# Performance work log

Measured on AMD Instinct MI355X. Metric: run time of the kernel, lower is better.

Reference implementation:

```python
import jax, jax.numpy as jnp
import numpy as np

N = 50          # n_nodes
TAU = 1.0       # sinkhorn_tau
ITERS = 5       # sinkhorn_iters
ALPHA = 1.0


def _psi_fn(x, W1, b1, W2, b2):
    # x: [B, N, F]
    h = jax.nn.leaky_relu(x @ W1 + b1)          # [B, N, H], slope 0.01 matches torch default
    M = jax.nn.leaky_relu(h @ W2 + b2)          # [B, N, N]
    P = jnp.exp(M / TAU)
    for _ in range(ITERS):                      # alternating row/col normalization
        P = P / jnp.sum(P, axis=2, keepdims=True)
        P = P / jnp.sum(P, axis=1, keepdims=True)
    return P


def _hungarian(cost):
    """O(n^3) Hungarian (shortest augmenting path, like scipy.linear_sum_assignment).
    cost: [n, n] numpy. Returns col index assigned to each row (minimizes cost)."""
    n = cost.shape[0]
    INF = 1e18
    u = np.zeros(n + 1)
    v = np.zeros(n + 1)
    p = np.zeros(n + 1, dtype=np.int64)   # p[j] = row matched to column j (1-based)
    for i in range(1, n + 1):
        p[0] = i
        j0 = 0
        minv = np.full(n + 1, INF)
        way = np.zeros(n + 1, dtype=np.int64)
        used = np.zeros(n + 1, dtype=bool)
        while True:
            used[j0] = True
            i0 = p[j0]
            cur = cost[i0 - 1, :] - u[i0] - v[1:]
            free = ~used[1:]
            better = free & (cur < minv[1:])
            mv = minv[1:]
            mv[better] = cur[better]
            way[1:][better] = j0
            cand = np.where(free, mv, INF)
            j1 = int(np.argmin(cand)) + 1
            delta = cand[j1 - 1]
            u[p[used]] += delta
            v[used] -= delta
            mv[free] -= delta
            j0 = j1
            if p[j0] == 0:
                break
        while j0 != 0:
            j1 = way[j0]
            p[j0] = p[j1]
            j0 = j1
    row_to_col = np.zeros(n, dtype=np.int64)
    for j in range(1, n + 1):
        if p[j] > 0:
            row_to_col[p[j] - 1] = j - 1
    return row_to_col


def setup_inputs() -> dict:
    key = jax.random.key(0)
    k1, k2, k3, k4, k5 = jax.random.split(key, 5)
    B, F, H = 128, 1024, 4096
    s1 = 1.0 / np.sqrt(F)
    s2 = 1.0 / np.sqrt(H)
    x = jax.random.normal(k1, (B, N, F), dtype=jnp.float32)
    W1 = jax.random.uniform(k2, (F, H), minval=-s1, maxval=s1, dtype=jnp.float32)
    b1 = jax.random.uniform(k3, (H,), minval=-s1, maxval=s1, dtype=jnp.float32)
    W2 = jax.random.uniform(k4, (H, N), minval=-s2, maxval=s2, dtype=jnp.float32)
    b2 = jax.random.uniform(k5, (N,), minval=-s2, maxval=s2, dtype=jnp.float32)
    return {"x": x, "W1": W1, "b1": b1, "W2": W2, "b2": b2, "do_round": 1}


def reference(x, W1, b1, W2, b2, do_round):
    psi = _psi_fn(x, W1, b1, W2, b2)            # [B, N, N] doubly-stochastic (approx)
    if do_round:
        batch = np.asarray(psi)
        B = batch.shape[0]
        perms_np = np.zeros((B, N, N), dtype=np.float32)
        rows = np.arange(N)
        for i in range(B):
            cols = _hungarian(-batch[i])        # maximize psi == minimize -psi
            perms_np[i, rows, cols] = 1.0
        perms = jnp.asarray(perms_np)
        dist = jnp.sum(psi * perms, axis=(1, 2)) / N   # [B]
        X = (1.0 - ALPHA) * perms + ALPHA * psi
        return (psi, perms, X, dist)
    return (psi, None, None, None)
```

## Files before the change

kernel.cpp:

```cpp
#include <hip/hip_runtime.h>

#define NMAT 50
#define BATCH 128
#define FDIM 1024
#define HDIM 4096
#define ROWS 6400
#define PSIZE 320000
#define NPART 32
#define HINF 1e18

#define WS_M_OFF   0
#define WS_XH_OFF  40960000LL
#define WS_XL_OFF  54067200LL
#define WS_W1H_OFF 67174400LL
#define WS_W1L_OFF 75563008LL
#define WS_W2H_OFF 83951616LL
#define WS_W2L_OFF 84475904LL
#define WS_H_OFF   85000192LL
#define WS_MIN     (WS_H_OFF + 128LL * HDIM * 4)

typedef __bf16 bf16x8 __attribute__((ext_vector_type(8)));
typedef short short8 __attribute__((ext_vector_type(8)));
typedef float f32x4 __attribute__((ext_vector_type(4)));
typedef unsigned short u16;
typedef unsigned int u32;

__device__ __forceinline__ float bf16_to_f32(unsigned short h) {
  return __uint_as_float(((unsigned int)h) << 16);
}
__device__ __forceinline__ unsigned short f32_to_bf16(float f) {
  unsigned int u = __float_as_uint(f);
  u += 0x7FFFu + ((u >> 16) & 1u);
  return (unsigned short)(u >> 16);
}

__device__ __forceinline__ void gload16(const u16* g, u16* l) {
  __builtin_amdgcn_global_load_lds(
      (const __attribute__((address_space(1))) unsigned int*)g,
      (__attribute__((address_space(3))) unsigned int*)l, 16, 0, 0);
}

__device__ __forceinline__ double wave_min_f64(double x) {
  union { double d; int i[2]; } u, t;
  u.d = x;
#define DPP_MIN_STEP(ctrl)                                                   \
  t.i[0] = __builtin_amdgcn_update_dpp(u.i[0], u.i[0], ctrl, 0xf, 0xf, false);\
  t.i[1] = __builtin_amdgcn_update_dpp(u.i[1], u.i[1], ctrl, 0xf, 0xf, false);\
  u.d = fmin(u.d, t.d);
  DPP_MIN_STEP(0x111)
  DPP_MIN_STEP(0x112)
  DPP_MIN_STEP(0x114)
  DPP_MIN_STEP(0x118)
  DPP_MIN_STEP(0x142)
  DPP_MIN_STEP(0x143)
#undef DPP_MIN_STEP
  union { double d; int i[2]; } r;
  r.i[0] = __builtin_amdgcn_readlane(u.i[0], 63);
  r.i[1] = __builtin_amdgcn_readlane(u.i[1], 63);
  return r.d;
}

__device__ __forceinline__ float wave_min_f32(float x) {
  float t;
#define DPP_MINF_STEP(ctrl)                                                  \
  t = __uint_as_float(__builtin_amdgcn_update_dpp(                           \
      (int)__float_as_uint(x), (int)__float_as_uint(x), ctrl, 0xf, 0xf, false));\
  x = fminf(x, t);
  DPP_MINF_STEP(0x111)
  DPP_MINF_STEP(0x112)
  DPP_MINF_STEP(0x114)
  DPP_MINF_STEP(0x118)
  DPP_MINF_STEP(0x142)
  DPP_MINF_STEP(0x143)
#undef DPP_MINF_STEP
  return __uint_as_float(__builtin_amdgcn_readlane((int)__float_as_uint(x), 63));
}

__device__ __forceinline__ double readlane_f64(double x, int l) {
  union { double d; int i2[2]; } a, b;
  a.d = x;
  b.i2[0] = __builtin_amdgcn_readlane(a.i2[0], l);
  b.i2[1] = __builtin_amdgcn_readlane(a.i2[1], l);
  return b.d;
}

__global__ __launch_bounds__(256) void convert_all(
    const float* __restrict__ X, u16* __restrict__ Xh, u16* __restrict__ Xl,
    const float* __restrict__ W1, u16* __restrict__ W1h, u16* __restrict__ W1l,
    const float* __restrict__ W2, u16* __restrict__ W2h, u16* __restrict__ W2l) {
  int b = blockIdx.x, t = threadIdx.x;
  if (b < 1600) {
    int mt = b >> 5, k0b = b & 31;
    size_t outbase = (size_t)b * 4096;
#pragma unroll
    for (int it = 0; it < 2; ++it) {
      int idx = t + it * 256;
      int m = idx & 127, kg = idx >> 7;
      const float* src = X + (size_t)(mt * 128 + m) * FDIM + k0b * 32 + kg * 8;
      float4 v0 = *(const float4*)src;
      float4 v1 = *(const float4*)(src + 4);
      float f[8] = {v0.x, v0.y, v0.z, v0.w, v1.x, v1.y, v1.z, v1.w};
      unsigned short h[8], l[8];
#pragma unroll
      for (int j = 0; j < 8; ++j) {
        h[j] = f32_to_bf16(f[j]);
        l[j] = f32_to_bf16(f[j] - bf16_to_f32(h[j]));
      }
      uint4 hv, lv;
      hv.x = h[0] | ((unsigned)h[1] << 16); hv.y = h[2] | ((unsigned)h[3] << 16);
      hv.z = h[4] | ((unsigned)h[5] << 16); hv.w = h[6] | ((unsigned)h[7] << 16);
      lv.x = l[0] | ((unsigned)l[1] << 16); lv.y = l[2] | ((unsigned)l[3] << 16);
      lv.z = l[4] | ((unsigned)l[5] << 16); lv.w = l[6] | ((unsigned)l[7] << 16);
      size_t off = outbase + (size_t)(kg * 128 + m) * 8;
      *(uint4*)&Xh[off] = hv;
      *(uint4*)&Xl[off] = lv;
    }
  } else if (b < 2624) {
    int bx = b - 1600;
    int nt = bx >> 5, k0b = bx & 31;
    size_t outbase = (size_t)bx * 4096;
#pragma unroll
    for (int it = 0; it < 2; ++it) {
      int idx = t + it * 256;
      int n = idx & 127, kg = idx >> 7;
      float f[8];
#pragma unroll
      for (int j = 0; j < 8; ++j)
        f[j] = W1[(size_t)(k0b * 32 + kg * 8 + j) * HDIM + nt * 128 + n];
      unsigned short h[8], l[8];
#pragma unroll
      for (int j = 0; j < 8; ++j) {
        h[j] = f32_to_bf16(f[j]);
        l[j] = f32_to_bf16(f[j] - bf16_to_f32(h[j]));
      }
      uint4 hv, lv;
      hv.x = h[0] | ((unsigned)h[1] << 16); hv.y = h[2] | ((unsigned)h[3] << 16);
      hv.z = h[4] | ((unsigned)h[5] << 16); hv.w = h[6] | ((unsigned)h[7] << 16);
      lv.x = l[0] | ((unsigned)l[1] << 16); lv.y = l[2] | ((unsigned)l[3] << 16);
      lv.z = l[4] | ((unsigned)l[5] << 16); lv.w = l[6] | ((unsigned)l[7] << 16);
      size_t off = outbase + (size_t)(kg * 128 + n) * 8;
      *(uint4*)&W1h[off] = hv;
      *(uint4*)&W1l[off] = lv;
    }
  } else {
    int idx = (b - 2624) * 256 + t;
    int n = idx >> 12, k = idx & 4095;
    float f = (n < NMAT) ? W2[(size_t)k * NMAT + n] : 0.0f;
    unsigned short hi = f32_to_bf16(f);
    unsigned short lo = f32_to_bf16(f - bf16_to_f32(hi));
    W2h[idx] = hi;
    W2l[idx] = lo;
  }
}

__global__ __launch_bounds__(256) void gemm1_mfma(
    const u16* __restrict__ Ah_, const u16* __restrict__ Al_,
    const u16* __restrict__ Bh_, const u16* __restrict__ Bl_,
    const float* __restrict__ b1,
    u32* __restrict__ HTout,
    int mt0, int stride) {
  __shared__ __align__(16) u16 Ah[4096];
  __shared__ __align__(16) u16 Al[4096];
  __shared__ __align__(16) u16 Bh[4096];
  __shared__ __align__(16) u16 Bl[4096];
  int t = threadIdx.x;
  int wave = t >> 6, lane = t & 63;
  int nt = blockIdx.x & 31;
  int mtl = blockIdx.x >> 5;
  int wm = wave >> 1, wn = wave & 1;
  int fr = lane & 15, fg = lane >> 4;

  f32x4 acc[4][4];
#pragma unroll
  for (int i = 0; i < 4; ++i)
#pragma unroll
    for (int j = 0; j < 4; ++j) acc[i][j] = (f32x4){0.f, 0.f, 0.f, 0.f};

  const u16* pAh = Ah_ + (size_t)(mt0 + mtl) * 32 * 4096;
  const u16* pAl = Al_ + (size_t)(mt0 + mtl) * 32 * 4096;
  const u16* pBh = Bh_ + (size_t)nt * 32 * 4096;
  const u16* pBl = Bl_ + (size_t)nt * 32 * 4096;
  int so = wave * 1024 + lane * 8;
  int ld = wave * 1024;

  for (int k0b = 0; k0b < 32; ++k0b) {
    __syncthreads();
    size_t sb = (size_t)k0b * 4096;
    gload16(pAh + sb + so,       &Ah[ld]);
    gload16(pAh + sb + so + 512, &Ah[ld + 512]);
    gload16(pAl + sb + so,       &Al[ld]);
    gload16(pAl + sb + so + 512, &Al[ld + 512]);
    gload16(pBh + sb + so,       &Bh[ld]);
    gload16(pBh + sb + so + 512, &Bh[ld + 512]);
    gload16(pBl + sb + so,       &Bl[ld]);
    gload16(pBl + sb + so + 512, &Bl[ld + 512]);
    __syncthreads();
    bf16x8 ah[4], al[4], bh[4], bl[4];
#pragma unroll
    for (int i = 0; i < 4; ++i) {
      int arow = (fg * 128 + wm * 64 + i * 16 + fr) * 8;
      ah[i] = *(const bf16x8*)&Ah[arow];
      al[i] = *(const bf16x8*)&Al[arow];
      int brow = (fg * 128 + wn * 64 + i * 16 + fr) * 8;
      bh[i] = *(const bf16x8*)&Bh[brow];
      bl[i] = *(const bf16x8*)&Bl[brow];
    }
#pragma unroll
    for (int i = 0; i < 4; ++i)
#pragma unroll
      for (int j = 0; j < 4; ++j)
        acc[i][j] = __builtin_amdgcn_mfma_f32_16x16x32_bf16(ah[i], bh[j], acc[i][j], 0, 0, 0);
#pragma unroll
    for (int i = 0; i < 4; ++i)
#pragma unroll
      for (int j = 0; j < 4; ++j)
        acc[i][j] = __builtin_amdgcn_mfma_f32_16x16x32_bf16(ah[i], bl[j], acc[i][j], 0, 0, 0);
#pragma unroll
    for (int i = 0; i < 4; ++i)
#pragma unroll
      for (int j = 0; j < 4; ++j)
        acc[i][j] = __builtin_amdgcn_mfma_f32_16x16x32_bf16(al[i], bh[j], acc[i][j], 0, 0, 0);
  }

  int colb = nt * 128 + wn * 64 + fr;
  int rowb = mtl * 128 + wm * 64 + fg * 4;
#pragma unroll
  for (int j = 0; j < 4; ++j) {
    float bias = b1[colb + j * 16];
#pragma unroll
    for (int i = 0; i < 4; ++i) {
      uint4 pk;
      u32* pp = &pk.x;
#pragma unroll
      for (int r = 0; r < 4; ++r) {
        float v = acc[i][j][r] + bias;
        v = v >= 0.0f ? v : 0.01f * v;
        unsigned short hi = f32_to_bf16(v);
        unsigned short lo = f32_to_bf16(v - bf16_to_f32(hi));
        pp[r] = ((u32)hi << 16) | lo;
      }
      *(uint4*)&HTout[(size_t)(colb + j * 16) * stride + rowb + i * 16] = pk;
    }
  }
}

__global__ __launch_bounds__(64) void gemm2_bf16(
    const u32* __restrict__ hT,
    const u16* __restrict__ W2h,
    const u16* __restrict__ W2l,
    float* __restrict__ Mpart,
    int row0, int stride) {
  int lane = threadIdx.x;
  int kz = blockIdx.y;
  int fr = lane & 15, fg = lane >> 4;

  f32x4 acc[4];
#pragma unroll
  for (int nt = 0; nt < 4; ++nt) acc[nt] = (f32x4){0.f, 0.f, 0.f, 0.f};

  const u32* hA = hT + blockIdx.x * 16 + fr;
  const int kbase = kz * 128;
  u32 hp[8], hn[8];
#pragma unroll
  for (int kk = 0; kk < 8; ++kk)
    hp[kk] = hA[(size_t)(kbase + fg * 8 + kk) * stride];
#pragma unroll
  for (int kk = 0; kk < 8; ++kk)
    hn[kk] = hA[(size_t)(kbase + 32 + fg * 8 + kk) * stride];

  for (int ks = 0; ks < 4; ++ks) {
    int k0 = kbase + ks * 32;
    u32 h2[8];
    if (ks < 2) {
#pragma unroll
      for (int kk = 0; kk < 8; ++kk)
        h2[kk] = hA[(size_t)(k0 + 64 + fg * 8 + kk) * stride];
    }
    short8 hs, ls;
#pragma unroll
    for (int kk = 0; kk < 8; ++kk) {
      hs[kk] = (short)(hp[kk] >> 16);
      ls[kk] = (short)(hp[kk] & 0xffffu);
    }
    bf16x8 ah = *(bf16x8*)&hs;
    bf16x8 al = *(bf16x8*)&ls;
#pragma unroll
    for (int nt = 0; nt < 4; ++nt) {
      const size_t boff = (size_t)(nt * 16 + fr) * 4096 + k0 + fg * 8;
      bf16x8 bh = *(const bf16x8*)&W2h[boff];
      bf16x8 bl = *(const bf16x8*)&W2l[boff];
      acc[nt] = __builtin_amdgcn_mfma_f32_16x16x32_bf16(ah, bh, acc[nt], 0, 0, 0);
      acc[nt] = __builtin_amdgcn_mfma_f32_16x16x32_bf16(ah, bl, acc[nt], 0, 0, 0);
      acc[nt] = __builtin_amdgcn_mfma_f32_16x16x32_bf16(al, bh, acc[nt], 0, 0, 0);
    }
    if (ks < 3) {
#pragma unroll
      for (int kk = 0; kk < 8; ++kk) hp[kk] = hn[kk];
    }
    if (ks < 2) {
#pragma unroll
      for (int kk = 0; kk < 8; ++kk) hn[kk] = h2[kk];
    }
  }

  float* Mout = Mpart + (size_t)kz * PSIZE;
  int rowbase = row0 + blockIdx.x * 16 + fg * 4;
#pragma unroll
  for (int nt = 0; nt < 4; ++nt) {
    int col = nt * 16 + fr;
    if (col < NMAT) {
#pragma unroll
      for (int r = 0; r < 4; ++r)
        Mout[(size_t)(rowbase + r) * NMAT + col] = acc[nt][r];
    }
  }
}

__global__ __launch_bounds__(256) void merge_m(
    const float* __restrict__ Mpart, double* __restrict__ Mmerged) {
  int idx = blockIdx.x * 256 + threadIdx.x;
  double s = 0.0;
#pragma unroll
  for (int pz = 0; pz < NPART; ++pz)
    s += (double)Mpart[(size_t)pz * PSIZE + idx];
  Mmerged[idx] = s;
}

__global__ __launch_bounds__(64) void sinkhorn_hungarian(
    const double* __restrict__ Mm, const float* __restrict__ b2,
    float* __restrict__ out_psi, float* __restrict__ out_X,
    float* __restrict__ out_perms, float* __restrict__ out_dist) {
  int b = blockIdx.x, lane = threadIdx.x;
  __shared__ double P[2500];
  __shared__ double rs[50];
  __shared__ double u[51];
  __shared__ int p[51];
  __shared__ int wayl[51];
  const size_t base = (size_t)b * 2500;

  for (int e = lane; e < 2500; e += 64) {
    double m = Mm[base + e] + (double)b2[e % 50];
    m = m >= 0.0 ? m : 0.01 * m;
    P[e] = exp(m);
  }
  __syncthreads();
  for (int it = 0; it < 5; ++it) {
    if (lane < 50) { double s = 0; for (int j = 0; j < 50; ++j) s += P[lane * 50 + j]; rs[lane] = s; }
    __syncthreads();
    for (int e = lane; e < 2500; e += 64) P[e] /= rs[e / 50];
    __syncthreads();
    if (lane < 50) { double s = 0; for (int r = 0; r < 50; ++r) s += P[r * 50 + lane]; rs[lane] = s; }
    __syncthreads();
    for (int e = lane; e < 2500; e += 64) P[e] /= rs[e % 50];
    __syncthreads();
  }
  for (int e = lane; e < 2500; e += 64) {
    float f = (float)P[e];
    out_psi[base + e] = f;
    out_X[base + e] = f;
  }
  if (lane < 51) { u[lane] = 0.0; p[lane] = 0; }
  __syncthreads();

  double v = 0.0;
  bool lactive = lane < NMAT;
  for (int i = 1; i <= NMAT; ++i) {
    int pc = (lane <= 50) ? p[lane] : 0;
    double uc = (lane < 50) ? u[lane + 1] : 0.0;
    bool used = false;
    int way = 0;
    int j0 = 0, j1 = 0;
    double uacc = 0.0, total = 0.0;
    for (int guard = 0; guard < 64; ++guard) {
      if (lane == j0 - 1) used = true;
      int j0u = __builtin_amdgcn_readfirstlane(j0);
      int i0 = (j0u == 0) ? i : __builtin_amdgcn_readlane(pc, j0u);
      double ui0 = readlane_f64(uc, i0 - 1);
      double cand = HINF;
      if (lactive && !used) {
        cand = -P[(i0 - 1) * NMAT + lane] - ui0 - v;
        way = j0;
      }
      float cf = (float)cand;
      float mf = wave_min_f32(cf);
      unsigned long long balf = __ballot(cf == mf);
      double m;
      if (__builtin_popcountll(balf) == 1) {
        int lmin = (int)__builtin_ctzll(balf);
        m = readlane_f64(cand, lmin);
        j1 = lmin + 1;
      } else {
        double candt = (cf == mf) ? cand : HINF;
        m = wave_min_f64(candt);
        unsigned long long bal = __ballot(cand == m);
        j1 = (int)__builtin_ctzll(bal) + 1;
      }
      if (used) { v -= m; uacc += m; }
      total += m;
      j0 = j1;
      int j1u = __builtin_amdgcn_readfirstlane(j0);
      if (__builtin_amdgcn_readlane(pc, j1u) == 0) break;
    }
    if (used && lactive) u[p[lane + 1]] += uacc;
    if (lane == 63) u[i] += total;
    if (lactive) wayl[lane + 1] = way;
    __syncthreads();
    if (lane == 0) {
      int j = j1;
      for (int step = 0; step < 64 && j != 0; ++step) {
        int jw = wayl[j];
        p[j] = (jw == 0) ? i : p[jw];
        j = jw;
      }
    }
    __syncthreads();
  }

  size_t pbase = (size_t)b * 2500;
  for (int e = lane; e < 2500; e += 64) out_perms[pbase + e] = 0.0f;
  __syncthreads();
  double val = 0.0;
  if (lactive) {
    int row = p[lane + 1] - 1;
    if (row < 0) row = 0;
    if (row > 49) row = 49;
    out_perms[pbase + (size_t)row * NMAT + lane] = 1.0f;
    val = P[(size_t)row * NMAT + lane];
  }
#pragma unroll
  for (int s = 32; s > 0; s >>= 1) val += __shfl_xor(val, s, 64);
  if (lane == 0) out_dist[b] = (float)(val / (double)NMAT);
}

extern "C" void kernel_launch(void* const* d_in, const int* in_sizes, int n_in,
                              void* d_out, int out_size, void* d_ws, size_t ws_size,
                              hipStream_t stream) {
  const float* x  = (const float*)d_in[0];
  const float* W1 = (const float*)d_in[1];
  const float* b1 = (const float*)d_in[2];
  const float* W2 = (const float*)d_in[3];
  const float* b2 = (const float*)d_in[4];
  float* out = (float*)d_out;
  float* out_psi   = out;
  float* out_perms = out + PSIZE;
  float* out_X     = out + 2 * PSIZE;
  float* out_dist  = out + 3 * PSIZE;

  if (ws_size < (size_t)WS_MIN) return;

  char* ws = (char*)d_ws;
  float* Mpart = (float*)(ws + WS_M_OFF);
  u16* Xh  = (u16*)(ws + WS_XH_OFF);
  u16* Xl  = (u16*)(ws + WS_XL_OFF);
  u16* W1h = (u16*)(ws + WS_W1H_OFF);
  u16* W1l = (u16*)(ws + WS_W1L_OFF);
  u16* W2h = (u16*)(ws + WS_W2H_OFF);
  u16* W2l = (u16*)(ws + WS_W2L_OFF);
  u32* hbuf = (u32*)(ws + WS_H_OFF);
  double* Mmerged = (double*)(ws + WS_H_OFF);
  long long avail = (long long)ws_size - WS_H_OFF;
  int max_rows = (int)(avail / (HDIM * 4));
  max_rows = (max_rows / 128) * 128;
  if (max_rows > ROWS) max_rows = ROWS;

  hipLaunchKernelGGL(convert_all, dim3(3648), dim3(256), 0, stream,
                     x, Xh, Xl, W1, W1h, W1l, W2, W2h, W2l);

  for (int r0 = 0; r0 < ROWS; r0 += max_rows) {
    int rows = (ROWS - r0 < max_rows) ? (ROWS - r0) : max_rows;
    hipLaunchKernelGGL(gemm1_mfma, dim3((rows / 128) * 32), dim3(256), 0, stream,
                       Xh, Xl, W1h, W1l, b1, hbuf, r0 / 128, rows);
    hipLaunchKernelGGL(gemm2_bf16, dim3(rows / 16, NPART), dim3(64), 0, stream,
                       hbuf, W2h, W2l, Mpart, r0, rows);
  }
  hipLaunchKernelGGL(merge_m, dim3(1250), dim3(256), 0, stream, Mpart, Mmerged);
  hipLaunchKernelGGL(sinkhorn_hungarian, dim3(BATCH), dim3(64), 0, stream,
                     Mmerged, b2, out_psi, out_X, out_perms, out_dist);
}
```

Measured before the change: 457.2 us.

## Enlarge gemm1 block tile to 256x128 with 512 threads sharing W1 tile

The first GEMM now has each block compute two 128-row M tiles (256 rows) against one 128-column W1 tile, using 512 threads and a single unified 48KB LDS buffer. Each thread precomputes global source pointers for six 16-byte chunks. The aim is to halve W1 tile reloads per output and reduce global/L2 traffic. In exchange the block count halves and LDS and thread use per block go up, which may lower occupancy. Workspace minimum and row-chunking are adjusted to multiples of 256.

```diff
diff --git a/kernel.cpp b/kernel.cpp
--- a/kernel.cpp
+++ b/kernel.cpp
@@ -17,7 +17,7 @@
 #define WS_W2H_OFF 83951616LL
 #define WS_W2L_OFF 84475904LL
 #define WS_H_OFF   85000192LL
-#define WS_MIN     (WS_H_OFF + 128LL * HDIM * 4)
+#define WS_MIN     (WS_H_OFF + 256LL * HDIM * 4)
 
 typedef __bf16 bf16x8 __attribute__((ext_vector_type(8)));
 typedef short short8 __attribute__((ext_vector_type(8)));
@@ -153,22 +153,41 @@
   }
 }
 
-__global__ __launch_bounds__(256) void gemm1_mfma(
-    const u16* __restrict__ Ah_, const u16* __restrict__ Al_,
-    const u16* __restrict__ Bh_, const u16* __restrict__ Bl_,
+__global__ __launch_bounds__(512) void gemm1_mfma(
+    const u16* __restrict__ Xh_, const u16* __restrict__ Xl_,
+    const u16* __restrict__ W1h_, const u16* __restrict__ W1l_,
     const float* __restrict__ b1,
     u32* __restrict__ HTout,
     int mt0, int stride) {
-  __shared__ __align__(16) u16 Ah[4096];
-  __shared__ __align__(16) u16 Al[4096];
-  __shared__ __align__(16) u16 Bh[4096];
-  __shared__ __align__(16) u16 Bl[4096];
+  __shared__ __align__(16) u16 S[24576];
   int t = threadIdx.x;
   int wave = t >> 6, lane = t & 63;
   int nt = blockIdx.x & 31;
   int mtl = blockIdx.x >> 5;
   int wm = wave >> 1, wn = wave & 1;
   int fr = lane & 15, fg = lane >> 4;
+  int MT0 = mt0 + 2 * mtl;
+
+  const u16* pre[6];
+#pragma unroll
+  for (int c = 0; c < 6; ++c) {
+    int flat = c * 4096 + t * 8;
+    const u16* base;
+    if (flat < 16384) {
+      int w = flat & 8191;
+      int kg = w >> 11, m = (w >> 3) & 255;
+      const u16* plane = (flat < 8192) ? Xh_ : Xl_;
+      base = plane + (size_t)((MT0 + (m >> 7)) * 32) * 4096 + kg * 1024 +
+             (m & 127) * 8;
+    } else {
+      int w = (flat - 16384) & 4095;
+      int kg = w >> 10, n = (w >> 3) & 127;
+      const u16* plane = (flat < 20480) ? W1h_ : W1l_;
+      base = plane + (size_t)(nt * 32) * 4096 + kg * 1024 + n * 8;
+    }
+    pre[c] = base;
+  }
+  int ldsb = wave * 512;
 
   f32x4 acc[4][4];
 #pragma unroll
@@ -176,34 +195,22 @@
 #pragma unroll
     for (int j = 0; j < 4; ++j) acc[i][j] = (f32x4){0.f, 0.f, 0.f, 0.f};
 
-  const u16* pAh = Ah_ + (size_t)(mt0 + mtl) * 32 * 4096;
-  const u16* pAl = Al_ + (size_t)(mt0 + mtl) * 32 * 4096;
-  const u16* pBh = Bh_ + (size_t)nt * 32 * 4096;
-  const u16* pBl = Bl_ + (size_t)nt * 32 * 4096;
-  int so = wave * 1024 + lane * 8;
-  int ld = wave * 1024;
-
   for (int k0b = 0; k0b < 32; ++k0b) {
     __syncthreads();
     size_t sb = (size_t)k0b * 4096;
-    gload16(pAh + sb + so,       &Ah[ld]);
-    gload16(pAh + sb + so + 512, &Ah[ld + 512]);
-    gload16(pAl + sb + so,       &Al[ld]);
-    gload16(pAl + sb + so + 512, &Al[ld + 512]);
-    gload16(pBh + sb + so,       &Bh[ld]);
-    gload16(pBh + sb + so + 512, &Bh[ld + 512]);
-    gload16(pBl + sb + so,       &Bl[ld]);
-    gload16(pBl + sb + so + 512, &Bl[ld + 512]);
+#pragma unroll
+    for (int c = 0; c < 6; ++c)
+      gload16(pre[c] + sb, &S[c * 4096 + ldsb]);
     __syncthreads();
     bf16x8 ah[4], al[4], bh[4], bl[4];
 #pragma unroll
     for (int i = 0; i < 4; ++i) {
-      int arow = (fg * 128 + wm * 64 + i * 16 + fr) * 8;
-      ah[i] = *(const bf16x8*)&Ah[arow];
-      al[i] = *(const bf16x8*)&Al[arow];
-      int brow = (fg * 128 + wn * 64 + i * 16 + fr) * 8;
-      bh[i] = *(const bf16x8*)&Bh[brow];
-      bl[i] = *(const bf16x8*)&Bl[brow];
+      int arow = fg * 2048 + (wm * 64 + i * 16 + fr) * 8;
+      ah[i] = *(const bf16x8*)&S[arow];
+      al[i] = *(const bf16x8*)&S[8192 + arow];
+      int brow = fg * 1024 + (wn * 64 + i * 16 + fr) * 8;
+      bh[i] = *(const bf16x8*)&S[16384 + brow];
+      bl[i] = *(const bf16x8*)&S[20480 + brow];
     }
 #pragma unroll
     for (int i = 0; i < 4; ++i)
@@ -223,7 +230,7 @@
   }
 
   int colb = nt * 128 + wn * 64 + fr;
-  int rowb = mtl * 128 + wm * 64 + fg * 4;
+  int rowb = mtl * 256 + wm * 64 + fg * 4;
 #pragma unroll
   for (int j = 0; j < 4; ++j) {
     float bias = b1[colb + j * 16];
@@ -460,7 +467,7 @@
   double* Mmerged = (double*)(ws + WS_H_OFF);
   long long avail = (long long)ws_size - WS_H_OFF;
   int max_rows = (int)(avail / (HDIM * 4));
-  max_rows = (max_rows / 128) * 128;
+  max_rows = (max_rows / 256) * 256;
   if (max_rows > ROWS) max_rows = ROWS;
 
   hipLaunchKernelGGL(convert_all, dim3(3648), dim3(256), 0, stream,
@@ -468,7 +475,7 @@
 
   for (int r0 = 0; r0 < ROWS; r0 += max_rows) {
     int rows = (ROWS - r0 < max_rows) ? (ROWS - r0) : max_rows;
-    hipLaunchKernelGGL(gemm1_mfma, dim3((rows / 128) * 32), dim3(256), 0, stream,
+    hipLaunchKernelGGL(gemm1_mfma, dim3((rows / 256) * 32), dim3(512), 0, stream,
                        Xh, Xl, W1h, W1l, b1, hbuf, r0 / 128, rows);
     hipLaunchKernelGGL(gemm2_bf16, dim3(rows / 16, NPART), dim3(64), 0, stream,
                        hbuf, W2h, W2l, Mpart, r0, rows);
```

Result: no change. 450.9 us (-1.4%).
